# Kernel tuning notes

Measured on AMD Instinct MI355X. Metric: run time of the kernel, lower is better.

## Reference

```python
import jax, jax.numpy as jnp
import numpy as np

DIM = 4096
N_HEADS = 32
N_KV_HEADS = 8
HEAD_DIM = 128
N_REP = N_HEADS // N_KV_HEADS  # 4
Q_DIM = N_HEADS * HEAD_DIM     # 4096
K_DIM = N_KV_HEADS * HEAD_DIM  # 1024
B, T = 2, 2048
ROPE_THETA = 10000.0


def setup_inputs() -> dict:
    key = jax.random.key(0)
    k1, k2, k3, k4 = jax.random.split(key, 4)
    x = jax.random.normal(k1, (B, T, DIM), dtype=jnp.float32)
    wqkv = jax.random.normal(k2, (Q_DIM + 2 * K_DIM, DIM), dtype=jnp.float32) * 0.02
    wo = jax.random.normal(k3, (DIM, DIM), dtype=jnp.float32) * 0.02
    # RoPE tables: [max_T, head_dim//2]
    inv_freq = 1.0 / (ROPE_THETA ** (jnp.arange(0, HEAD_DIM, 2, dtype=jnp.float32) / HEAD_DIM))
    angles = jnp.arange(T, dtype=jnp.float32)[:, None] * inv_freq[None, :]  # [T, D/2]
    cos = jnp.cos(angles)
    sin = jnp.sin(angles)
    freqs_cis = jax.random.normal(k4, (T, HEAD_DIM // 2), dtype=jnp.float32)  # unused by forward
    return {"x": x, "freqs_cis": freqs_cis, "wqkv": wqkv, "wo": wo, "cos": cos, "sin": sin}


def _apply_rope(q, k, cos, sin):
    # q: [B,T,Hq,D], k: [B,T,Hkv,D]; interleaved even/odd pairs
    Tlen = q.shape[1]
    c = cos[:Tlen][None, :, None, :]  # [1,T,1,D/2]
    s = sin[:Tlen][None, :, None, :]

    def rot(t):
        tr, ti = t[..., 0::2], t[..., 1::2]
        or_ = tr * c - ti * s
        oi = tr * s + ti * c
        return jnp.stack([or_, oi], axis=-1).reshape(t.shape)

    return rot(q), rot(k)


def reference(x, freqs_cis, wqkv, wo, cos, sin):
    Bx, Tx, _ = x.shape
    qkv = jnp.einsum('btd,ed->bte', x, wqkv)  # fused QKV GEMM
    q = qkv[..., :Q_DIM].reshape(Bx, Tx, N_HEADS, HEAD_DIM)
    k = qkv[..., Q_DIM:Q_DIM + K_DIM].reshape(Bx, Tx, N_KV_HEADS, HEAD_DIM)
    v = qkv[..., Q_DIM + K_DIM:].reshape(Bx, Tx, N_KV_HEADS, HEAD_DIM)
    q, k = _apply_rope(q, k, cos, sin)
    # GQA repeat_interleave over head dim
    k = jnp.repeat(k, N_REP, axis=2)  # [B,T,Hq,D]
    v = jnp.repeat(v, N_REP, axis=2)
    scale = 1.0 / jnp.sqrt(jnp.asarray(HEAD_DIM, dtype=q.dtype))
    scores = jnp.einsum('bqhd,bkhd->bhqk', q, k) * scale  # [B,H,T,T]
    causal = jnp.tril(jnp.ones((Tx, Tx), dtype=bool))
    scores = jnp.where(causal[None, None], scores, jnp.finfo(scores.dtype).min)
    probs = jax.nn.softmax(scores, axis=-1)
    y = jnp.einsum('bhqk,bkhd->bqhd', probs, v).reshape(Bx, Tx, Q_DIM)
    return jnp.einsum('btd,ed->bte', y, wo)
```

## Files before the change

kernel.cpp:

```cpp
#include <hip/hip_runtime.h>

#define T_SEQ 2048
#define NB    2
#define NH    32
#define NKV   8
#define HD    128
#define DIM   4096
#define EDIM  6144
#define M_TOK 4096

typedef __bf16          bf8  __attribute__((ext_vector_type(8)));
typedef unsigned short  us8  __attribute__((ext_vector_type(8)));
typedef float           f4   __attribute__((ext_vector_type(4)));
typedef float           f16v __attribute__((ext_vector_type(16)));
typedef int             i4   __attribute__((ext_vector_type(4)));

__device__ inline unsigned short f2bf(float f) {
  unsigned int u = __builtin_bit_cast(unsigned int, f);
  u += 0x7FFF + ((u >> 16) & 1);
  return (unsigned short)(u >> 16);
}
__device__ inline float bf2f(unsigned short h) {
  unsigned int u = ((unsigned int)h) << 16;
  return __builtin_bit_cast(float, u);
}
__device__ inline void gl_lds16(const void* g, void* l) {
  __builtin_amdgcn_global_load_lds(
      (const __attribute__((address_space(1))) unsigned int*)g,
      (__attribute__((address_space(3))) unsigned int*)l, 16, 0, 0);
}
__device__ inline f4 mfma16(bf8 a, bf8 b, f4 c) {
  return __builtin_amdgcn_mfma_f32_16x16x32_bf16(a, b, c, 0, 0, 0);
}
__device__ inline f16v mfma32(bf8 a, bf8 b, f16v c) {
  return __builtin_amdgcn_mfma_f32_32x32x16_bf16(a, b, c, 0, 0, 0);
}
__device__ inline unsigned cvtpk(float lo, float hi) {
  unsigned r;
  asm("v_cvt_pk_bf16_f32 %0, %1, %2" : "=v"(r) : "v"(lo), "v"(hi));
  return r;
}

__global__ void k_f2bf(const float* __restrict__ in, unsigned short* __restrict__ out, int n4) {
  int i = blockIdx.x * blockDim.x + threadIdx.x;
  if (i >= n4) return;
  f4 v = *(const f4*)(in + (size_t)i * 4);
  unsigned long long pack =
      (unsigned long long)f2bf(v[0]) |
      ((unsigned long long)f2bf(v[1]) << 16) |
      ((unsigned long long)f2bf(v[2]) << 32) |
      ((unsigned long long)f2bf(v[3]) << 48);
  *(unsigned long long*)(out + (size_t)i * 4) = pack;
}


#define MFMA_Q(a0, b0, AF, BF)                                        \
  __builtin_amdgcn_s_setprio(1);                                      \
  _Pragma("unroll") for (int mi = 0; mi < 4; ++mi)                    \
  _Pragma("unroll") for (int ni = 0; ni < 2; ++ni)                    \
  _Pragma("unroll") for (int kk = 0; kk < 2; ++kk)                    \
      acc[(a0) + mi][(b0) + ni] =                                     \
          mfma16(AF[mi][kk], BF[ni][kk], acc[(a0) + mi][(b0) + ni]);  \
  __builtin_amdgcn_s_setprio(0);

#define RD_A(buf, mh)                                                 \
  _Pragma("unroll") for (int mi = 0; mi < 4; ++mi)                    \
  _Pragma("unroll") for (int kk = 0; kk < 2; ++kk)                    \
      af[mi][kk] = rdA(buf, mh, mi, kk);

#define RD_B(buf, nh, BF)                                             \
  _Pragma("unroll") for (int ni = 0; ni < 2; ++ni)                    \
  _Pragma("unroll") for (int kk = 0; kk < 2; ++kk)                    \
      BF[ni][kk] = rdB(buf, nh, ni, kk);

template <int MODE>
__global__ __launch_bounds__(512, 2)
void k_gemm256(const unsigned short* __restrict__ A, const unsigned short* __restrict__ Bm,
               int M, int N, int K,
               unsigned short* __restrict__ oQ, unsigned short* __restrict__ oK,
               unsigned short* __restrict__ oV, float* __restrict__ oF) {
  __shared__ unsigned short As[2][16384];
  __shared__ unsigned short Bs[2][16384];
  const int nbx = N >> 8;
  const int nwg = nbx * (M >> 8);
  {
  }
  const int n0 = blockIdx.x;
  const int q8 = nwg >> 3, r8 = nwg & 7;
  const int xcd = n0 & 7, ix = n0 >> 3;
  const int swzb = (xcd < r8 ? xcd * (q8 + 1) : r8 * (q8 + 1) + (xcd - r8) * q8) + ix;
  const int bn = swzb % nbx, bm = swzb / nbx;
  const int t = threadIdx.x;
  const int lane = t & 63, w = t >> 6;
  const int wr = w >> 2, wc = w & 3;
  const int l15 = lane & 15, lhi = lane >> 4;
  const int KT = K >> 6;
  const int NI = KT >> 1;

  f4 acc[8][4] = {};

  const int tt0 = t * 8;
  auto stA = [&](int buf, int half, int tile) {
    if (tile >= KT) return;
    const unsigned short* gp = A + (size_t)(bm * 256 + half * 128) * K + tile * 64;
#pragma unroll
    for (int j = 0; j < 2; ++j) {
      int e = j * 4096 + tt0;
      int rl = e >> 6;
      int cs = (e & 63) ^ ((rl & 7) << 3);
      gl_lds16(gp + (size_t)rl * K + cs, &As[buf][half * 8192 + e]);
    }
  };
  auto stB = [&](int buf, int half, int tile) {
    if (tile >= KT) return;
    const unsigned short* gp = Bm + (size_t)(bn * 256 + half * 128) * K + tile * 64;
#pragma unroll
    for (int j = 0; j < 2; ++j) {
      int e = j * 4096 + tt0;
      int rl = e >> 6;
      int cs = (e & 63) ^ ((rl & 7) << 3);
      gl_lds16(gp + (size_t)rl * K + cs, &Bs[buf][half * 8192 + e]);
    }
  };
  auto rdA = [&](int buf, int mh, int mi, int kk) -> bf8 {
    int row = mh * 128 + wr * 64 + mi * 16 + l15;
    int col = (lhi * 8 + kk * 32) ^ ((row & 7) << 3);
    return __builtin_bit_cast(bf8, *(const us8*)&As[buf][row * 64 + col]);
  };
  auto rdB = [&](int buf, int nh, int ni, int kk) -> bf8 {
    int row = nh * 128 + wc * 32 + ni * 16 + l15;
    int col = (lhi * 8 + kk * 32) ^ ((row & 7) << 3);
    return __builtin_bit_cast(bf8, *(const us8*)&Bs[buf][row * 64 + col]);
  };
  auto bar = [&]() {
    asm volatile("" ::: "memory");
    __builtin_amdgcn_s_barrier();
    asm volatile("" ::: "memory");
  };
  auto lgkm0 = [&]() {
    asm volatile("s_waitcnt lgkmcnt(0)" ::: "memory");
    __builtin_amdgcn_sched_barrier(0);
  };

  stA(0, 0, 0); stB(0, 1, 0); stA(0, 1, 0); stB(0, 0, 0);
  stA(1, 0, 1); stB(1, 1, 1); stA(1, 1, 1);
  asm volatile("s_waitcnt vmcnt(6)" ::: "memory");
  bar();

  for (int i = 0; i < NI; ++i) {
    const int t2 = 2 * i + 2, t3 = 2 * i + 3;
    bf8 af[4][2], bf0[2][2], bf1[2][2];
    RD_A(0, 0); RD_B(0, 0, bf0);
    stB(1, 0, 2 * i + 1);
    bar(); lgkm0();
    MFMA_Q(0, 0, af, bf0);
    bar();
    RD_B(0, 1, bf1);
    stA(0, 0, t2);
    bar(); lgkm0();
    MFMA_Q(0, 2, af, bf1);
    bar();
    RD_A(0, 1);
    stB(0, 1, t2);
    bar(); lgkm0();
    MFMA_Q(4, 2, af, bf1);
    bar();
    RD_B(0, 0, bf0);
    stA(0, 1, t2);
    bar(); lgkm0();
    MFMA_Q(4, 0, af, bf0);
    if (i + 1 < NI) { asm volatile("s_waitcnt vmcnt(6)" ::: "memory"); }
    else            { asm volatile("s_waitcnt vmcnt(0)" ::: "memory"); }
    bar();
    RD_A(1, 0); RD_B(1, 0, bf0);
    stB(0, 0, t2);
    bar(); lgkm0();
    MFMA_Q(0, 0, af, bf0);
    bar();
    RD_B(1, 1, bf1);
    stA(1, 0, t3);
    bar(); lgkm0();
    MFMA_Q(0, 2, af, bf1);
    bar();
    RD_A(1, 1);
    stB(1, 1, t3);
    bar(); lgkm0();
    MFMA_Q(4, 2, af, bf1);
    bar();
    RD_B(1, 0, bf0);
    stA(1, 1, t3);
    bar(); lgkm0();
    MFMA_Q(4, 0, af, bf0);
    if (i + 1 < NI) { asm volatile("s_waitcnt vmcnt(6)" ::: "memory"); }
    bar();
  }

  const int rb0 = bm * 256 + wr * 64 + lhi * 4;
  const int cb0 = bn * 256 + wc * 32 + l15;
  if (MODE == 0) {
    unsigned short* op; int ldo, coff;
    const int cbase = bn * 256;
    if (cbase < 4096)      { op = oQ; ldo = 4096; coff = cb0; }
    else if (cbase < 5120) { op = oK; ldo = 1024; coff = cb0 - 4096; }
    else                   { op = oV; ldo = 1024; coff = cb0 - 5120; }
#pragma unroll
    for (int ai = 0; ai < 8; ++ai)
#pragma unroll
      for (int bj = 0; bj < 4; ++bj)
#pragma unroll
        for (int rr = 0; rr < 4; ++rr) {
          int row = rb0 + (ai >> 2) * 128 + (ai & 3) * 16 + rr;
          int col = coff + (bj >> 1) * 128 + (bj & 1) * 16;
          op[(size_t)row * ldo + col] = f2bf(acc[ai][bj][rr]);
        }
  } else {
#pragma unroll
    for (int ai = 0; ai < 8; ++ai)
#pragma unroll
      for (int bj = 0; bj < 4; ++bj)
#pragma unroll
        for (int rr = 0; rr < 4; ++rr) {
          int row = rb0 + (ai >> 2) * 128 + (ai & 3) * 16 + rr;
          int col = cb0 + (bj >> 1) * 128 + (bj & 1) * 16;
          oF[(size_t)row * N + col] = acc[ai][bj][rr];
        }
  }
}

__global__ void k_rope(unsigned short* __restrict__ Qb, unsigned short* __restrict__ Kb,
                       const float* __restrict__ cosp, const float* __restrict__ sinp) {
  const float QSCALE = (float)(0.08838834764831845 * 1.4426950408889634);
  int idx = blockIdx.x * blockDim.x + threadIdx.x;
  const int nq = M_TOK * NH * 16;
  const int nk = M_TOK * NKV * 16;
  unsigned short* p; int tpos, pg; float sc;
  if (idx < nq) {
    int m = idx >> 9;
    int r = idx & 511;
    int h = r >> 4; pg = r & 15;
    tpos = m & (T_SEQ - 1);
    p = Qb + (size_t)m * 4096 + h * 128 + pg * 8;
    sc = QSCALE;
  } else {
    idx -= nq;
    if (idx >= nk) return;
    int m = idx >> 7;
    int r = idx & 127;
    int h = r >> 4; pg = r & 15;
    tpos = m & (T_SEQ - 1);
    p = Kb + (size_t)m * 1024 + h * 128 + pg * 8;
    sc = 1.0f;
  }
  us8 v = *(const us8*)p;
  f4 c = *(const f4*)(cosp + tpos * 64 + pg * 4);
  f4 s = *(const f4*)(sinp + tpos * 64 + pg * 4);
  us8 o;
#pragma unroll
  for (int j = 0; j < 4; ++j) {
    float cs = c[j] * sc, ss = s[j] * sc;
    float tr = bf2f(v[2 * j]), ti = bf2f(v[2 * j + 1]);
    o[2 * j]     = f2bf(tr * cs - ti * ss);
    o[2 * j + 1] = f2bf(tr * ss + ti * cs);
  }
  *(us8*)p = o;
}

__global__ __launch_bounds__(512, 2)
void k_attn(const unsigned short* __restrict__ Qb, const unsigned short* __restrict__ Kb,
            const unsigned short* __restrict__ Vb, unsigned short* __restrict__ Yb) {
  __shared__ unsigned short Ks[64 * 128];
  __shared__ unsigned short Vt[128 * 64];
  const int idx = blockIdx.x;
  const int qblk = 7 - (idx >> 6);
  const int h = (idx & 63) >> 1;
  const int b = idx & 1;
  const int kvh = h >> 2;
  const int t = threadIdx.x;
  const int lane = t & 63, w = t >> 6;
  const int l31 = lane & 31, hh = lane >> 5;
  const int qb0 = qblk * 256;
  const int NT = (qblk + 1) * 4;
  const int wqmin = qb0 + w * 32;
  const int q_g = wqmin + l31;
  const float BNEG = -1.0e30f;

  bf8 qf[8];
  {
    const unsigned short* qp = Qb + (size_t)(b * T_SEQ + q_g) * 4096 + h * 128 + hh * 8;
#pragma unroll
    for (int st = 0; st < 8; ++st) qf[st] = __builtin_bit_cast(bf8, *(const us8*)(qp + st * 16));
  }
  const int swz = (l31 & 7) << 3;
  float m_run = BNEG, l_run = 0.f;
  f16v yacc[4] = {};

  const int eo0 = t * 8;
  for (int kt = 0; kt < NT; ++kt) {
    const int kbase = kt * 64;
    const unsigned short* vp = Vb + (size_t)(b * T_SEQ + kbase + lane) * 1024 + kvh * 128 + w * 8;
    us8 vv0 = *(const us8*)vp;
    us8 vv1 = *(const us8*)(vp + 64);
    __syncthreads();
#pragma unroll
    for (int i = 0; i < 2; ++i) {
      int eo = i * 4096 + eo0;
      int row = eo >> 7;
      int colL = (eo & 127) ^ ((row & 7) << 3);
      gl_lds16(Kb + (size_t)(b * T_SEQ + kbase + row) * 1024 + kvh * 128 + colL, &Ks[eo]);
    }
#pragma unroll
    for (int j = 0; j < 8; ++j) {
      int d0 = w * 8 + j;
      Vt[(d0 * 64 + lane) ^ ((d0 & 7) << 3)] = vv0[j];
      int d1 = d0 + 64;
      Vt[(d1 * 64 + lane) ^ ((d1 & 7) << 3)] = vv1[j];
    }
    __syncthreads();
    if (kbase > wqmin + 31) continue;

    f16v s0 = {}, s1 = {};
#pragma unroll
    for (int st = 0; st < 8; ++st) {
      int coff = st * 16 + hh * 8;
      bf8 a0 = __builtin_bit_cast(bf8, *(const us8*)&Ks[(l31 * 128 + coff) ^ swz]);
      bf8 a1 = __builtin_bit_cast(bf8, *(const us8*)&Ks[((l31 + 32) * 128 + coff) ^ swz]);
      s0 = mfma32(a0, qf[st], s0);
      s1 = mfma32(a1, qf[st], s1);
    }
    if (kbase + 63 > wqmin) {
#pragma unroll
      for (int r = 0; r < 16; ++r) {
        int kv = kbase + (r & 3) + 8 * (r >> 2) + 4 * hh;
        if (kv > q_g)      s0[r] = BNEG;
        if (kv + 32 > q_g) s1[r] = BNEG;
      }
    }
    float tmax = BNEG;
#pragma unroll
    for (int r = 0; r < 16; ++r) {
      tmax = fmaxf(tmax, s0[r]);
      tmax = fmaxf(tmax, s1[r]);
    }
    tmax = fmaxf(tmax, __shfl_xor(tmax, 32));
    float m_new = fmaxf(m_run, tmax);
    float fac = exp2f(m_run - m_new);
    m_run = m_new;
    float psum = 0.f;
#pragma unroll
    for (int r = 0; r < 16; ++r) {
      s0[r] = exp2f(s0[r] - m_new); psum += s0[r];
      s1[r] = exp2f(s1[r] - m_new); psum += s1[r];
    }
    psum += __shfl_xor(psum, 32);
    l_run = l_run * fac + psum;
    if (!__all(fac == 1.0f)) {
      float facr[16];
#pragma unroll
      for (int r = 0; r < 16; ++r)
        facr[r] = __shfl(fac, (r & 3) + 8 * (r >> 2) + 4 * hh);
#pragma unroll
      for (int dc = 0; dc < 4; ++dc)
#pragma unroll
        for (int r = 0; r < 16; ++r) yacc[dc][r] *= facr[r];
    }
#pragma unroll
    for (int st = 0; st < 4; ++st) {
      f16v sv = (st & 2) ? s1 : s0;
      const int rb = (st & 1) * 8;
      unsigned pkA = cvtpk(sv[rb + 0], sv[rb + 1]);
      unsigned pkB = cvtpk(sv[rb + 2], sv[rb + 3]);
      unsigned pkC = cvtpk(sv[rb + 4], sv[rb + 5]);
      unsigned pkD = cvtpk(sv[rb + 6], sv[rb + 7]);
      unsigned xA = __shfl_xor(pkA, 32);
      unsigned xB = __shfl_xor(pkB, 32);
      unsigned xC = __shfl_xor(pkC, 32);
      unsigned xD = __shfl_xor(pkD, 32);
      unsigned w0 = hh ? xC : pkA;
      unsigned w1 = hh ? xD : pkB;
      unsigned w2 = hh ? pkC : xA;
      unsigned w3 = hh ? pkD : xB;
      i4 wi = { (int)w0, (int)w1, (int)w2, (int)w3 };
      bf8 pf = __builtin_bit_cast(bf8, wi);
#pragma unroll
      for (int dc = 0; dc < 4; ++dc) {
        int d = dc * 32 + l31;
        bf8 vf = __builtin_bit_cast(bf8, *(const us8*)&Vt[(d * 64 + st * 16 + hh * 8) ^ swz]);
        yacc[dc] = mfma32(pf, vf, yacc[dc]);
      }
    }
  }
  float inv_l = 1.0f / l_run;
  float il[16];
#pragma unroll
  for (int r = 0; r < 16; ++r)
    il[r] = __shfl(inv_l, (r & 3) + 8 * (r >> 2) + 4 * hh);
#pragma unroll
  for (int dc = 0; dc < 4; ++dc)
#pragma unroll
    for (int r = 0; r < 16; ++r) {
      int qrow = qb0 + w * 32 + (r & 3) + 8 * (r >> 2) + 4 * hh;
      Yb[(size_t)(b * T_SEQ + qrow) * 4096 + h * 128 + dc * 32 + l31] =
          f2bf(yacc[dc][r] * il[r]);
    }
}

extern "C" void kernel_launch(void* const* d_in, const int* in_sizes, int n_in,
                              void* d_out, int out_size, void* d_ws, size_t ws_size,
                              hipStream_t stream) {
  const float* x    = (const float*)d_in[0];
  const float* wqkv = (const float*)d_in[2];
  const float* wo   = (const float*)d_in[3];
  const float* cosp = (const float*)d_in[4];
  const float* sinp = (const float*)d_in[5];
  float* out = (float*)d_out;

  char* ws = (char*)d_ws;
  size_t o = 0;
  auto alloc = [&](size_t bytes) { void* p = ws + o; o += (bytes + 255) & ~(size_t)255; return p; };
  unsigned short* x_b    = (unsigned short*)alloc((size_t)M_TOK * DIM * 2);
  unsigned short* wqkv_b = (unsigned short*)alloc((size_t)EDIM * DIM * 2);
  unsigned short* wo_b   = (unsigned short*)alloc((size_t)DIM * DIM * 2);
  unsigned short* Qb     = (unsigned short*)alloc((size_t)M_TOK * 4096 * 2);
  unsigned short* Kb     = (unsigned short*)alloc((size_t)M_TOK * 1024 * 2);
  unsigned short* Vb     = (unsigned short*)alloc((size_t)M_TOK * 1024 * 2);
  unsigned short* Yb     = (unsigned short*)alloc((size_t)M_TOK * 4096 * 2);
  if (o > ws_size) return;

  k_f2bf<<<(M_TOK * DIM / 4 + 255) / 256, 256, 0, stream>>>(x, x_b, M_TOK * DIM / 4);
  k_f2bf<<<(EDIM * DIM / 4 + 255) / 256, 256, 0, stream>>>(wqkv, wqkv_b, EDIM * DIM / 4);
  k_f2bf<<<(DIM * DIM / 4 + 255) / 256, 256, 0, stream>>>(wo, wo_b, DIM * DIM / 4);

  k_gemm256<0><<<dim3((EDIM / 256) * (M_TOK / 256)), 512, 0, stream>>>(
      x_b, wqkv_b, M_TOK, EDIM, DIM, Qb, Kb, Vb, nullptr);

  k_rope<<<(M_TOK * NH * 16 + M_TOK * NKV * 16 + 255) / 256, 256, 0, stream>>>(
      Qb, Kb, cosp, sinp);

  k_attn<<<dim3(512, 1, 1), 512, 0, stream>>>(Qb, Kb, Vb, Yb);

  k_gemm256<1><<<dim3((DIM / 256) * (M_TOK / 256)), 512, 0, stream>>>(
      Yb, wo_b, M_TOK, DIM, DIM, nullptr, nullptr, nullptr, out);
}
```

Baseline: 529.1 us.

## Switch GEMMs to 32x32x16 MFMA, drop redundant B reload, fuse casts

The 256x256 GEMM kernel moves from 16x16x32 to 32x32x16 bf16 MFMA tiles, which changes the LDS fragment read pattern, the accumulator layout and the epilogue store mapping. The fourth quarter of each k-step now reuses the B fragments already held in registers instead of reading them from LDS again, so one LDS read phase and its wait are removed. The three fp32-to-bf16 conversion launches become a single grid-stride kernel, which saves launch overhead. The larger MFMA shape means fewer instructions and fewer LDS reads per FLOP, at the cost of more live registers to hold the bf0 fragments across phases.

```diff
diff --git a/kernel.cpp b/kernel.cpp
--- a/kernel.cpp
+++ b/kernel.cpp
@@ -29,9 +29,6 @@
       (const __attribute__((address_space(1))) unsigned int*)g,
       (__attribute__((address_space(3))) unsigned int*)l, 16, 0, 0);
 }
-__device__ inline f4 mfma16(bf8 a, bf8 b, f4 c) {
-  return __builtin_amdgcn_mfma_f32_16x16x32_bf16(a, b, c, 0, 0, 0);
-}
 __device__ inline f16v mfma32(bf8 a, bf8 b, f16v c) {
   return __builtin_amdgcn_mfma_f32_32x32x16_bf16(a, b, c, 0, 0, 0);
 }
@@ -41,37 +38,47 @@
   return r;
 }
 
-__global__ void k_f2bf(const float* __restrict__ in, unsigned short* __restrict__ out, int n4) {
-  int i = blockIdx.x * blockDim.x + threadIdx.x;
-  if (i >= n4) return;
-  f4 v = *(const f4*)(in + (size_t)i * 4);
-  unsigned long long pack =
-      (unsigned long long)f2bf(v[0]) |
-      ((unsigned long long)f2bf(v[1]) << 16) |
-      ((unsigned long long)f2bf(v[2]) << 32) |
-      ((unsigned long long)f2bf(v[3]) << 48);
-  *(unsigned long long*)(out + (size_t)i * 4) = pack;
-}
-
-
-#define MFMA_Q(a0, b0, AF, BF)                                        \
+__global__ void k_f2bf3(const float* __restrict__ x, const float* __restrict__ wq,
+                        const float* __restrict__ wo,
+                        unsigned short* __restrict__ xb, unsigned short* __restrict__ wqb,
+                        unsigned short* __restrict__ wob) {
+  const long n0 = (long)M_TOK * DIM / 4;
+  const long n1 = (long)EDIM * DIM / 4;
+  const long n2 = (long)DIM * DIM / 4;
+  const long total = n0 + n1 + n2;
+  const long stride = (long)gridDim.x * blockDim.x;
+  for (long i = (long)blockIdx.x * blockDim.x + threadIdx.x; i < total; i += stride) {
+    const float* in; unsigned short* out; long j = i;
+    if (j < n0)              { in = x;  out = xb; }
+    else if ((j -= n0) < n1) { in = wq; out = wqb; }
+    else       { j -= n1;      in = wo; out = wob; }
+    f4 v = *(const f4*)(in + j * 4);
+    unsigned long long pack =
+        (unsigned long long)f2bf(v[0]) |
+        ((unsigned long long)f2bf(v[1]) << 16) |
+        ((unsigned long long)f2bf(v[2]) << 32) |
+        ((unsigned long long)f2bf(v[3]) << 48);
+    *(unsigned long long*)(out + j * 4) = pack;
+  }
+}
+
+
+#define RD_A32(buf, mh)                                               \
+  _Pragma("unroll") for (int m32 = 0; m32 < 2; ++m32)                 \
+  _Pragma("unroll") for (int kk = 0; kk < 4; ++kk)                    \
+      af[m32][kk] = rdA32(buf, mh, m32, kk);
+
+#define RD_B32(buf, nh, BF)                                           \
+  _Pragma("unroll") for (int kk = 0; kk < 4; ++kk)                    \
+      BF[kk] = rdB32(buf, nh, kk);
+
+#define MFMA32_Q(mh, nh, BF)                                          \
   __builtin_amdgcn_s_setprio(1);                                      \
-  _Pragma("unroll") for (int mi = 0; mi < 4; ++mi)                    \
-  _Pragma("unroll") for (int ni = 0; ni < 2; ++ni)                    \
-  _Pragma("unroll") for (int kk = 0; kk < 2; ++kk)                    \
-      acc[(a0) + mi][(b0) + ni] =                                     \
-          mfma16(AF[mi][kk], BF[ni][kk], acc[(a0) + mi][(b0) + ni]);  \
+  _Pragma("unroll") for (int kk = 0; kk < 4; ++kk)                    \
+  _Pragma("unroll") for (int m32 = 0; m32 < 2; ++m32)                 \
+      acc32[(mh) * 2 + m32][nh] =                                     \
+          mfma32(af[m32][kk], BF[kk], acc32[(mh) * 2 + m32][nh]);     \
   __builtin_amdgcn_s_setprio(0);
-
-#define RD_A(buf, mh)                                                 \
-  _Pragma("unroll") for (int mi = 0; mi < 4; ++mi)                    \
-  _Pragma("unroll") for (int kk = 0; kk < 2; ++kk)                    \
-      af[mi][kk] = rdA(buf, mh, mi, kk);
-
-#define RD_B(buf, nh, BF)                                             \
-  _Pragma("unroll") for (int ni = 0; ni < 2; ++ni)                    \
-  _Pragma("unroll") for (int kk = 0; kk < 2; ++kk)                    \
-      BF[ni][kk] = rdB(buf, nh, ni, kk);
 
 template <int MODE>
 __global__ __launch_bounds__(512, 2)
@@ -83,8 +90,6 @@
   __shared__ unsigned short Bs[2][16384];
   const int nbx = N >> 8;
   const int nwg = nbx * (M >> 8);
-  {
-  }
   const int n0 = blockIdx.x;
   const int q8 = nwg >> 3, r8 = nwg & 7;
   const int xcd = n0 & 7, ix = n0 >> 3;
@@ -93,11 +98,11 @@
   const int t = threadIdx.x;
   const int lane = t & 63, w = t >> 6;
   const int wr = w >> 2, wc = w & 3;
-  const int l15 = lane & 15, lhi = lane >> 4;
+  const int l31 = lane & 31, hh = lane >> 5;
   const int KT = K >> 6;
   const int NI = KT >> 1;
 
-  f4 acc[8][4] = {};
+  f16v acc32[4][2] = {};
 
   const int tt0 = t * 8;
   auto stA = [&](int buf, int half, int tile) {
@@ -122,14 +127,14 @@
       gl_lds16(gp + (size_t)rl * K + cs, &Bs[buf][half * 8192 + e]);
     }
   };
-  auto rdA = [&](int buf, int mh, int mi, int kk) -> bf8 {
-    int row = mh * 128 + wr * 64 + mi * 16 + l15;
-    int col = (lhi * 8 + kk * 32) ^ ((row & 7) << 3);
+  auto rdA32 = [&](int buf, int mh, int m32, int kk) -> bf8 {
+    int row = mh * 128 + wr * 64 + m32 * 32 + l31;
+    int col = (kk * 16 + hh * 8) ^ ((row & 7) << 3);
     return __builtin_bit_cast(bf8, *(const us8*)&As[buf][row * 64 + col]);
   };
-  auto rdB = [&](int buf, int nh, int ni, int kk) -> bf8 {
-    int row = nh * 128 + wc * 32 + ni * 16 + l15;
-    int col = (lhi * 8 + kk * 32) ^ ((row & 7) << 3);
+  auto rdB32 = [&](int buf, int nh, int kk) -> bf8 {
+    int row = nh * 128 + wc * 32 + l31;
+    int col = (kk * 16 + hh * 8) ^ ((row & 7) << 3);
     return __builtin_bit_cast(bf8, *(const us8*)&Bs[buf][row * 64 + col]);
   };
   auto bar = [&]() {
@@ -149,82 +154,76 @@
 
   for (int i = 0; i < NI; ++i) {
     const int t2 = 2 * i + 2, t3 = 2 * i + 3;
-    bf8 af[4][2], bf0[2][2], bf1[2][2];
-    RD_A(0, 0); RD_B(0, 0, bf0);
+    bf8 af[2][4], bf0[4], bf1[4];
+    RD_A32(0, 0); RD_B32(0, 0, bf0);
     stB(1, 0, 2 * i + 1);
-    bar(); lgkm0();
-    MFMA_Q(0, 0, af, bf0);
-    bar();
-    RD_B(0, 1, bf1);
+    asm volatile("s_waitcnt lgkmcnt(8)" ::: "memory");
+    bar(); lgkm0();
+    MFMA32_Q(0, 0, bf0);
+    bar();
+    RD_B32(0, 1, bf1);
     stA(0, 0, t2);
     bar(); lgkm0();
-    MFMA_Q(0, 2, af, bf1);
-    bar();
-    RD_A(0, 1);
+    MFMA32_Q(0, 1, bf1);
+    bar();
+    RD_A32(0, 1);
     stB(0, 1, t2);
     bar(); lgkm0();
-    MFMA_Q(4, 2, af, bf1);
-    bar();
-    RD_B(0, 0, bf0);
+    MFMA32_Q(1, 1, bf1);
+    bar();
     stA(0, 1, t2);
-    bar(); lgkm0();
-    MFMA_Q(4, 0, af, bf0);
+    bar();
+    MFMA32_Q(1, 0, bf0);
     if (i + 1 < NI) { asm volatile("s_waitcnt vmcnt(6)" ::: "memory"); }
     else            { asm volatile("s_waitcnt vmcnt(0)" ::: "memory"); }
     bar();
-    RD_A(1, 0); RD_B(1, 0, bf0);
+    RD_A32(1, 0); RD_B32(1, 0, bf0);
     stB(0, 0, t2);
-    bar(); lgkm0();
-    MFMA_Q(0, 0, af, bf0);
-    bar();
-    RD_B(1, 1, bf1);
+    asm volatile("s_waitcnt lgkmcnt(8)" ::: "memory");
+    bar(); lgkm0();
+    MFMA32_Q(0, 0, bf0);
+    bar();
+    RD_B32(1, 1, bf1);
     stA(1, 0, t3);
     bar(); lgkm0();
-    MFMA_Q(0, 2, af, bf1);
-    bar();
-    RD_A(1, 1);
+    MFMA32_Q(0, 1, bf1);
+    bar();
+    RD_A32(1, 1);
     stB(1, 1, t3);
     bar(); lgkm0();
-    MFMA_Q(4, 2, af, bf1);
-    bar();
-    RD_B(1, 0, bf0);
+    MFMA32_Q(1, 1, bf1);
+    bar();
     stA(1, 1, t3);
-    bar(); lgkm0();
-    MFMA_Q(4, 0, af, bf0);
+    bar();
+    MFMA32_Q(1, 0, bf0);
     if (i + 1 < NI) { asm volatile("s_waitcnt vmcnt(6)" ::: "memory"); }
     bar();
   }
 
-  const int rb0 = bm * 256 + wr * 64 + lhi * 4;
-  const int cb0 = bn * 256 + wc * 32 + l15;
-  if (MODE == 0) {
-    unsigned short* op; int ldo, coff;
-    const int cbase = bn * 256;
-    if (cbase < 4096)      { op = oQ; ldo = 4096; coff = cb0; }
-    else if (cbase < 5120) { op = oK; ldo = 1024; coff = cb0 - 4096; }
-    else                   { op = oV; ldo = 1024; coff = cb0 - 5120; }
-#pragma unroll
-    for (int ai = 0; ai < 8; ++ai)
-#pragma unroll
-      for (int bj = 0; bj < 4; ++bj)
-#pragma unroll
-        for (int rr = 0; rr < 4; ++rr) {
-          int row = rb0 + (ai >> 2) * 128 + (ai & 3) * 16 + rr;
-          int col = coff + (bj >> 1) * 128 + (bj & 1) * 16;
-          op[(size_t)row * ldo + col] = f2bf(acc[ai][bj][rr]);
+#pragma unroll
+  for (int mb = 0; mb < 4; ++mb)
+#pragma unroll
+    for (int nh = 0; nh < 2; ++nh) {
+      const int gcolb = bn * 256 + nh * 128 + wc * 32;
+      const int growb = bm * 256 + (mb >> 1) * 128 + wr * 64 + (mb & 1) * 32;
+      if (MODE == 0) {
+        unsigned short* op; int ldo, c0;
+        if (gcolb < 4096)      { op = oQ; ldo = 4096; c0 = gcolb; }
+        else if (gcolb < 5120) { op = oK; ldo = 1024; c0 = gcolb - 4096; }
+        else                   { op = oV; ldo = 1024; c0 = gcolb - 5120; }
+#pragma unroll
+        for (int r = 0; r < 16; ++r) {
+          int row = growb + (r & 3) + 8 * (r >> 2) + 4 * hh;
+          op[(size_t)row * ldo + c0 + l31] = f2bf(acc32[mb][nh][r]);
         }
-  } else {
-#pragma unroll
-    for (int ai = 0; ai < 8; ++ai)
-#pragma unroll
-      for (int bj = 0; bj < 4; ++bj)
-#pragma unroll
-        for (int rr = 0; rr < 4; ++rr) {
-          int row = rb0 + (ai >> 2) * 128 + (ai & 3) * 16 + rr;
-          int col = cb0 + (bj >> 1) * 128 + (bj & 1) * 16;
-          oF[(size_t)row * N + col] = acc[ai][bj][rr];
+      } else {
+#pragma unroll
+        for (int r = 0; r < 16; ++r) {
+          int row = growb + (r & 3) + 8 * (r >> 2) + 4 * hh;
+          oF[(size_t)row * N + gcolb + l31] = acc32[mb][nh][r];
         }
-  }
+      }
+    }
 }
 
 __global__ void k_rope(unsigned short* __restrict__ Qb, unsigned short* __restrict__ Kb,
@@ -426,9 +425,7 @@
   unsigned short* Yb     = (unsigned short*)alloc((size_t)M_TOK * 4096 * 2);
   if (o > ws_size) return;
 
-  k_f2bf<<<(M_TOK * DIM / 4 + 255) / 256, 256, 0, stream>>>(x, x_b, M_TOK * DIM / 4);
-  k_f2bf<<<(EDIM * DIM / 4 + 255) / 256, 256, 0, stream>>>(wqkv, wqkv_b, EDIM * DIM / 4);
-  k_f2bf<<<(DIM * DIM / 4 + 255) / 256, 256, 0, stream>>>(wo, wo_b, DIM * DIM / 4);
+  k_f2bf3<<<2048, 256, 0, stream>>>(x, wqkv, wo, x_b, wqkv_b, wo_b);
 
   k_gemm256<0><<<dim3((EDIM / 256) * (M_TOK / 256)), 512, 0, stream>>>(
       x_b, wqkv_b, M_TOK, EDIM, DIM, Qb, Kb, Vb, nullptr);
```

Result: slower. 563.3 us (+6.5%).

## Use 128x384 tiles for QKV GEMM and merge bf16 conversions into one kernel

Applied to the files above, without the earlier changes.

Replaces the 256x256-tile QKV projection GEMM with a dedicated 128x384-tile kernel. The grid grows from 384 to 512 workgroups, which fills the GPU's compute units more evenly and improves wave balance. The three fp32-to-bf16 conversion launches become one grid-stride kernel, cutting launch overhead. It also adds partial lgkmcnt waits before barriers in the output GEMM. The trade-offs are less data reuse per tile in the new GEMM and a more intricate wait-count schedule.

```diff
diff --git a/kernel.cpp b/kernel.cpp
--- a/kernel.cpp
+++ b/kernel.cpp
@@ -41,18 +41,181 @@
   return r;
 }
 
-__global__ void k_f2bf(const float* __restrict__ in, unsigned short* __restrict__ out, int n4) {
-  int i = blockIdx.x * blockDim.x + threadIdx.x;
-  if (i >= n4) return;
-  f4 v = *(const f4*)(in + (size_t)i * 4);
-  unsigned long long pack =
-      (unsigned long long)f2bf(v[0]) |
-      ((unsigned long long)f2bf(v[1]) << 16) |
-      ((unsigned long long)f2bf(v[2]) << 32) |
-      ((unsigned long long)f2bf(v[3]) << 48);
-  *(unsigned long long*)(out + (size_t)i * 4) = pack;
-}
-
+__global__ void k_f2bf3(const float* __restrict__ x, const float* __restrict__ wq,
+                        const float* __restrict__ wo,
+                        unsigned short* __restrict__ xb, unsigned short* __restrict__ wqb,
+                        unsigned short* __restrict__ wob) {
+  const long n0 = (long)M_TOK * DIM / 4;
+  const long n1 = (long)EDIM * DIM / 4;
+  const long n2 = (long)DIM * DIM / 4;
+  const long total = n0 + n1 + n2;
+  const long stride = (long)gridDim.x * blockDim.x;
+  for (long i = (long)blockIdx.x * blockDim.x + threadIdx.x; i < total; i += stride) {
+    const float* in; unsigned short* out; long j = i;
+    if (j < n0)              { in = x;  out = xb; }
+    else if ((j -= n0) < n1) { in = wq; out = wqb; }
+    else       { j -= n1;      in = wo; out = wob; }
+    f4 v = *(const f4*)(in + j * 4);
+    unsigned long long pack =
+        (unsigned long long)f2bf(v[0]) |
+        ((unsigned long long)f2bf(v[1]) << 16) |
+        ((unsigned long long)f2bf(v[2]) << 32) |
+        ((unsigned long long)f2bf(v[3]) << 48);
+    *(unsigned long long*)(out + j * 4) = pack;
+  }
+}
+
+__global__ __launch_bounds__(512, 2)
+void k_gemm384(const unsigned short* __restrict__ A, const unsigned short* __restrict__ Bm,
+               unsigned short* __restrict__ oQ, unsigned short* __restrict__ oK,
+               unsigned short* __restrict__ oV) {
+  __shared__ unsigned short As[2][8192];
+  __shared__ unsigned short Bs[2][3][8192];
+  const int nbx = EDIM / 384;
+  const int nwg = nbx * (M_TOK / 128);
+  const int n0 = blockIdx.x;
+  const int q8 = nwg >> 3, r8 = nwg & 7;
+  const int xcd = n0 & 7, ix = n0 >> 3;
+  const int swzb = (xcd < r8 ? xcd * (q8 + 1) : r8 * (q8 + 1) + (xcd - r8) * q8) + ix;
+  const int bn = swzb % nbx, bm = swzb / nbx;
+  const int t = threadIdx.x;
+  const int lane = t & 63, w = t >> 6;
+  const int wr = w >> 2, wc = w & 3;
+  const int l15 = lane & 15, lhi = lane >> 4;
+  const int KT = DIM >> 6;
+
+  f4 acc[4][6] = {};
+
+  const int tt0 = t * 8;
+  auto stA = [&](int buf, int tile) {
+    if (tile >= KT) return;
+    const unsigned short* gp = A + (size_t)(bm * 128) * DIM + tile * 64;
+#pragma unroll
+    for (int j = 0; j < 2; ++j) {
+      int e = j * 4096 + tt0;
+      int rl = e >> 6, cs = (e & 63) ^ ((rl & 7) << 3);
+      gl_lds16(gp + (size_t)rl * DIM + cs, &As[buf][e]);
+    }
+  };
+  auto stB = [&](int buf, int bh, int tile) {
+    if (tile >= KT) return;
+    const unsigned short* gp = Bm + (size_t)(bn * 384 + bh * 128) * DIM + tile * 64;
+#pragma unroll
+    for (int j = 0; j < 2; ++j) {
+      int e = j * 4096 + tt0;
+      int rl = e >> 6, cs = (e & 63) ^ ((rl & 7) << 3);
+      gl_lds16(gp + (size_t)rl * DIM + cs, &Bs[buf][bh][e]);
+    }
+  };
+  auto rdA = [&](int buf, int mi, int kk) -> bf8 {
+    int row = wr * 64 + mi * 16 + l15;
+    int col = (lhi * 8 + kk * 32) ^ ((row & 7) << 3);
+    return __builtin_bit_cast(bf8, *(const us8*)&As[buf][row * 64 + col]);
+  };
+  auto rdB = [&](int buf, int bh, int ni, int kk) -> bf8 {
+    int row = wc * 32 + ni * 16 + l15;
+    int col = (lhi * 8 + kk * 32) ^ ((row & 7) << 3);
+    return __builtin_bit_cast(bf8, *(const us8*)&Bs[buf][bh][row * 64 + col]);
+  };
+  auto bar = [&]() {
+    asm volatile("" ::: "memory");
+    __builtin_amdgcn_s_barrier();
+    asm volatile("" ::: "memory");
+  };
+  auto lgkm0 = [&]() {
+    asm volatile("s_waitcnt lgkmcnt(0)" ::: "memory");
+    __builtin_amdgcn_sched_barrier(0);
+  };
+
+  stA(0, 0); stB(0, 0, 0); stB(0, 1, 0); stB(0, 2, 0);
+  asm volatile("s_waitcnt vmcnt(4)" ::: "memory");
+  bar();
+
+  for (int tp = 0; tp < KT; tp += 2) {
+#pragma unroll
+    for (int sub = 0; sub < 2; ++sub) {
+      const int tc = tp + sub, b = sub;
+      const bool last = (tc == KT - 1);
+      bf8 af[4][2], bfr[2][2];
+#pragma unroll
+      for (int mi = 0; mi < 4; ++mi)
+#pragma unroll
+        for (int kk = 0; kk < 2; ++kk) af[mi][kk] = rdA(b, mi, kk);
+#pragma unroll
+      for (int ni = 0; ni < 2; ++ni)
+#pragma unroll
+        for (int kk = 0; kk < 2; ++kk) bfr[ni][kk] = rdB(b, 0, ni, kk);
+      stA(b ^ 1, tc + 1); stB(b ^ 1, 0, tc + 1);
+      asm volatile("s_waitcnt lgkmcnt(8)" ::: "memory");
+      bar(); lgkm0();
+      __builtin_amdgcn_s_setprio(1);
+#pragma unroll
+      for (int mi = 0; mi < 4; ++mi)
+#pragma unroll
+        for (int ni = 0; ni < 2; ++ni)
+#pragma unroll
+          for (int kk = 0; kk < 2; ++kk)
+            acc[mi][ni] = mfma16(af[mi][kk], bfr[ni][kk], acc[mi][ni]);
+      __builtin_amdgcn_s_setprio(0);
+      if (last) { asm volatile("s_waitcnt vmcnt(2)" ::: "memory"); }
+      else      { asm volatile("s_waitcnt vmcnt(6)" ::: "memory"); }
+      bar();
+#pragma unroll
+      for (int ni = 0; ni < 2; ++ni)
+#pragma unroll
+        for (int kk = 0; kk < 2; ++kk) bfr[ni][kk] = rdB(b, 1, ni, kk);
+      stB(b ^ 1, 1, tc + 1);
+      bar(); lgkm0();
+      __builtin_amdgcn_s_setprio(1);
+#pragma unroll
+      for (int mi = 0; mi < 4; ++mi)
+#pragma unroll
+        for (int ni = 0; ni < 2; ++ni)
+#pragma unroll
+          for (int kk = 0; kk < 2; ++kk)
+            acc[mi][2 + ni] = mfma16(af[mi][kk], bfr[ni][kk], acc[mi][2 + ni]);
+      __builtin_amdgcn_s_setprio(0);
+      if (last) { asm volatile("s_waitcnt vmcnt(0)" ::: "memory"); }
+      else      { asm volatile("s_waitcnt vmcnt(6)" ::: "memory"); }
+      bar();
+#pragma unroll
+      for (int ni = 0; ni < 2; ++ni)
+#pragma unroll
+        for (int kk = 0; kk < 2; ++kk) bfr[ni][kk] = rdB(b, 2, ni, kk);
+      stB(b ^ 1, 2, tc + 1);
+      bar(); lgkm0();
+      __builtin_amdgcn_s_setprio(1);
+#pragma unroll
+      for (int mi = 0; mi < 4; ++mi)
+#pragma unroll
+        for (int ni = 0; ni < 2; ++ni)
+#pragma unroll
+          for (int kk = 0; kk < 2; ++kk)
+            acc[mi][4 + ni] = mfma16(af[mi][kk], bfr[ni][kk], acc[mi][4 + ni]);
+      __builtin_amdgcn_s_setprio(0);
+      if (!last) { asm volatile("s_waitcnt vmcnt(4)" ::: "memory"); }
+      bar();
+    }
+  }
+
+#pragma unroll
+  for (int bh = 0; bh < 3; ++bh)
+#pragma unroll
+    for (int ni = 0; ni < 2; ++ni) {
+      const int colb = bn * 384 + bh * 128 + wc * 32 + ni * 16;
+      unsigned short* op; int ldo, c0;
+      if (colb < 4096)      { op = oQ; ldo = 4096; c0 = colb; }
+      else if (colb < 5120) { op = oK; ldo = 1024; c0 = colb - 4096; }
+      else                  { op = oV; ldo = 1024; c0 = colb - 5120; }
+#pragma unroll
+      for (int mi = 0; mi < 4; ++mi)
+#pragma unroll
+        for (int rr = 0; rr < 4; ++rr) {
+          int row = bm * 128 + wr * 64 + mi * 16 + lhi * 4 + rr;
+          op[(size_t)row * ldo + c0 + l15] = f2bf(acc[mi][bh * 2 + ni][rr]);
+        }
+    }
+}
 
 #define MFMA_Q(a0, b0, AF, BF)                                        \
   __builtin_amdgcn_s_setprio(1);                                      \
@@ -73,18 +236,13 @@
   _Pragma("unroll") for (int kk = 0; kk < 2; ++kk)                    \
       BF[ni][kk] = rdB(buf, nh, ni, kk);
 
-template <int MODE>
 __global__ __launch_bounds__(512, 2)
-void k_gemm256(const unsigned short* __restrict__ A, const unsigned short* __restrict__ Bm,
-               int M, int N, int K,
-               unsigned short* __restrict__ oQ, unsigned short* __restrict__ oK,
-               unsigned short* __restrict__ oV, float* __restrict__ oF) {
+void k_gemm256f(const unsigned short* __restrict__ A, const unsigned short* __restrict__ Bm,
+                int M, int N, int K, float* __restrict__ oF) {
   __shared__ unsigned short As[2][16384];
   __shared__ unsigned short Bs[2][16384];
   const int nbx = N >> 8;
   const int nwg = nbx * (M >> 8);
-  {
-  }
   const int n0 = blockIdx.x;
   const int q8 = nwg >> 3, r8 = nwg & 7;
   const int xcd = n0 & 7, ix = n0 >> 3;
@@ -152,6 +310,7 @@
     bf8 af[4][2], bf0[2][2], bf1[2][2];
     RD_A(0, 0); RD_B(0, 0, bf0);
     stB(1, 0, 2 * i + 1);
+    asm volatile("s_waitcnt lgkmcnt(8)" ::: "memory");
     bar(); lgkm0();
     MFMA_Q(0, 0, af, bf0);
     bar();
@@ -174,6 +333,7 @@
     bar();
     RD_A(1, 0); RD_B(1, 0, bf0);
     stB(0, 0, t2);
+    asm volatile("s_waitcnt lgkmcnt(8)" ::: "memory");
     bar(); lgkm0();
     MFMA_Q(0, 0, af, bf0);
     bar();
@@ -197,34 +357,16 @@
 
   const int rb0 = bm * 256 + wr * 64 + lhi * 4;
   const int cb0 = bn * 256 + wc * 32 + l15;
-  if (MODE == 0) {
-    unsigned short* op; int ldo, coff;
-    const int cbase = bn * 256;
-    if (cbase < 4096)      { op = oQ; ldo = 4096; coff = cb0; }
-    else if (cbase < 5120) { op = oK; ldo = 1024; coff = cb0 - 4096; }
-    else                   { op = oV; ldo = 1024; coff = cb0 - 5120; }
-#pragma unroll
-    for (int ai = 0; ai < 8; ++ai)
-#pragma unroll
-      for (int bj = 0; bj < 4; ++bj)
-#pragma unroll
-        for (int rr = 0; rr < 4; ++rr) {
-          int row = rb0 + (ai >> 2) * 128 + (ai & 3) * 16 + rr;
-          int col = coff + (bj >> 1) * 128 + (bj & 1) * 16;
-          op[(size_t)row * ldo + col] = f2bf(acc[ai][bj][rr]);
-        }
-  } else {
-#pragma unroll
-    for (int ai = 0; ai < 8; ++ai)
-#pragma unroll
-      for (int bj = 0; bj < 4; ++bj)
-#pragma unroll
-        for (int rr = 0; rr < 4; ++rr) {
-          int row = rb0 + (ai >> 2) * 128 + (ai & 3) * 16 + rr;
-          int col = cb0 + (bj >> 1) * 128 + (bj & 1) * 16;
-          oF[(size_t)row * N + col] = acc[ai][bj][rr];
-        }
-  }
+#pragma unroll
+  for (int ai = 0; ai < 8; ++ai)
+#pragma unroll
+    for (int bj = 0; bj < 4; ++bj)
+#pragma unroll
+      for (int rr = 0; rr < 4; ++rr) {
+        int row = rb0 + (ai >> 2) * 128 + (ai & 3) * 16 + rr;
+        int col = cb0 + (bj >> 1) * 128 + (bj & 1) * 16;
+        oF[(size_t)row * N + col] = acc[ai][bj][rr];
+      }
 }
 
 __global__ void k_rope(unsigned short* __restrict__ Qb, unsigned short* __restrict__ Kb,
@@ -426,18 +568,14 @@
   unsigned short* Yb     = (unsigned short*)alloc((size_t)M_TOK * 4096 * 2);
   if (o > ws_size) return;
 
-  k_f2bf<<<(M_TOK * DIM / 4 + 255) / 256, 256, 0, stream>>>(x, x_b, M_TOK * DIM / 4);
-  k_f2bf<<<(EDIM * DIM / 4 + 255) / 256, 256, 0, stream>>>(wqkv, wqkv_b, EDIM * DIM / 4);
-  k_f2bf<<<(DIM * DIM / 4 + 255) / 256, 256, 0, stream>>>(wo, wo_b, DIM * DIM / 4);
-
-  k_gemm256<0><<<dim3((EDIM / 256) * (M_TOK / 256)), 512, 0, stream>>>(
-      x_b, wqkv_b, M_TOK, EDIM, DIM, Qb, Kb, Vb, nullptr);
+  k_f2bf3<<<2048, 256, 0, stream>>>(x, wqkv, wo, x_b, wqkv_b, wo_b);
+
+  k_gemm384<<<dim3(512), 512, 0, stream>>>(x_b, wqkv_b, Qb, Kb, Vb);
 
   k_rope<<<(M_TOK * NH * 16 + M_TOK * NKV * 16 + 255) / 256, 256, 0, stream>>>(
       Qb, Kb, cosp, sinp);
 
   k_attn<<<dim3(512, 1, 1), 512, 0, stream>>>(Qb, Kb, Vb, Yb);
 
-  k_gemm256<1><<<dim3((DIM / 256) * (M_TOK / 256)), 512, 0, stream>>>(
-      Yb, wo_b, M_TOK, DIM, DIM, nullptr, nullptr, nullptr, out);
-}
+  k_gemm256f<<<dim3(256), 512, 0, stream>>>(Yb, wo_b, M_TOK, DIM, DIM, out);
+}
```

New measurement: 528.3 us. Within noise of the previous version (-0.2%).
